# Kernel optimization log

Measured on AMD Instinct MI355X. Metric: run time of the kernel, lower is better.

## Reference

```python
import jax, jax.numpy as jnp
import numpy as np

L, B, D, V = 4096, 4, 512, 1000  # seq_len, batch, hidden_dim, index_dim


def setup_inputs() -> dict:
    key = jax.random.key(0)
    k0, k1, k2, k3, k4 = jax.random.split(key, 5)
    s_d = 1.0 / np.sqrt(D)
    return {
        "x": jax.random.normal(k0, (L, B, D), dtype=jnp.float32),
        # ctc_weight: nn.Linear(D, D)
        "Ww": jax.random.uniform(k1, (D, D), dtype=jnp.float32, minval=-s_d, maxval=s_d),
        "Wb": jax.random.uniform(k2, (D,), dtype=jnp.float32, minval=-s_d, maxval=s_d),
        # ctc_linear: nn.Linear(D, V)
        "Lw": jax.random.uniform(k3, (V, D), dtype=jnp.float32, minval=-s_d, maxval=s_d),
        "Lb": jax.random.uniform(k4, (V,), dtype=jnp.float32, minval=-s_d, maxval=s_d),
    }


def reference(x, Ww, Wb, Lw, Lb):
    # x: (L, B, D) -> (B, L, D)
    xb = jnp.transpose(x, (1, 0, 2))
    # ctc_weight(x): (B, L, D)
    wx = xb @ Ww.T + Wb
    # bmm(x, W(x)^T): (B, L, L) bilinear scores (no softmax)
    scores = jnp.einsum('bld,bmd->blm', xb, wx)
    # bmm(scores, x): (B, L, D)
    y = jnp.einsum('blm,bmd->bld', scores, xb)
    # ctc_linear + log_softmax over vocab
    logits = y @ Lw.T + Lb  # (B, L, V)
    out = jax.nn.log_softmax(logits, axis=2)
    # permute back to (L, B, V)
    return jnp.transpose(out, (1, 0, 2))
```

## Files before the change

### kernel.cpp

```cpp
#include <hip/hip_runtime.h>
#include <math.h>

#define L_ 4096
#define B_ 4
#define D_ 512
#define V_ 1000
#define VP 1024
#define BD 2048
#define OUT_BV 4000
#define NCH 8

typedef __attribute__((ext_vector_type(8))) short short8;
typedef __attribute__((ext_vector_type(4))) float f32x4;
typedef __attribute__((ext_vector_type(4))) short short4v;

__device__ __forceinline__ short f2bf(float f) {
  unsigned u = __float_as_uint(f);
  unsigned r = (u + 0x7FFFu + ((u >> 16) & 1u)) >> 16;
  return (short)r;
}
__device__ __forceinline__ float bf2f(short v) {
  return __uint_as_float(((unsigned)(unsigned short)v) << 16);
}

__global__ __launch_bounds__(256) void kPre(const float* __restrict__ x,
                                            const float* __restrict__ Wb,
                                            short* __restrict__ xbf,
                                            short* __restrict__ xT,
                                            float* __restrict__ s,
                                            float* __restrict__ c) {
  const int l0 = blockIdx.x * 64, d0 = blockIdx.y * 64, b = blockIdx.z;
  __shared__ short tile[64 * 72];
  const int tid = threadIdx.x;
  const int r = tid >> 2;
  const int q = tid & 3;
  const int c0 = q * 16;

  short sv[16];
  float cpart = 0.f;
  const float* src = x + (size_t)(l0 + r) * BD + b * D_ + d0 + c0;
#pragma unroll
  for (int qq = 0; qq < 4; ++qq) {
    float4 f = *(const float4*)(src + qq * 4);
    const float* wb = Wb + d0 + c0 + qq * 4;
    cpart += f.x * wb[0] + f.y * wb[1] + f.z * wb[2] + f.w * wb[3];
    sv[qq * 4 + 0] = f2bf(f.x); sv[qq * 4 + 1] = f2bf(f.y);
    sv[qq * 4 + 2] = f2bf(f.z); sv[qq * 4 + 3] = f2bf(f.w);
  }
  short* dst = xbf + ((size_t)b * L_ + l0 + r) * D_ + d0 + c0;
  *(short8*)(dst)     = *(short8*)(sv);
  *(short8*)(dst + 8) = *(short8*)(sv + 8);
#pragma unroll
  for (int i = 0; i < 16; ++i) tile[(c0 + i) * 72 + r] = sv[i];
  cpart += __shfl_xor(cpart, 1);
  cpart += __shfl_xor(cpart, 2);
  if (q == 0) atomicAdd(&c[b * L_ + l0 + r], cpart);
  __syncthreads();
  short8 t0 = *(const short8*)(tile + r * 72 + c0);
  short8 t1 = *(const short8*)(tile + r * 72 + c0 + 8);
  short* tdst = xT + ((size_t)b * D_ + d0 + r) * L_ + l0 + c0;
  *(short8*)(tdst)     = t0;
  *(short8*)(tdst + 8) = t1;
  float spart = 0.f;
#pragma unroll
  for (int i = 0; i < 8; ++i) spart += bf2f(t0[i]) + bf2f(t1[i]);
  spart += __shfl_xor(spart, 1);
  spart += __shfl_xor(spart, 2);
  if (q == 0) atomicAdd(&s[b * D_ + d0 + r], spart);
}

__global__ __launch_bounds__(256) void kT(const float* __restrict__ Lw,
                                          const float* __restrict__ s,
                                          float* __restrict__ t) {
  const int w = threadIdx.x >> 6, lane = threadIdx.x & 63;
  const int wid = blockIdx.x * 4 + w;
  const int b = wid >> 10, v = wid & 1023;
  float sum = 0.f;
  if (v < V_) {
    const float* lr = Lw + (size_t)v * D_;
    const float* sb = s + b * D_;
#pragma unroll
    for (int i = 0; i < 8; ++i) sum += lr[lane + i * 64] * sb[lane + i * 64];
  }
  for (int off = 32; off; off >>= 1) sum += __shfl_down(sum, off);
  if (lane == 0) t[b * VP + v] = (v < V_) ? sum : 0.f;
}

__global__ __launch_bounds__(256) void kGbf(const short* __restrict__ xT,
                                            short* __restrict__ Gpart) {
  const int z = blockIdx.z;
  const int b = z >> 3, ch = z & 7;
  const int i0 = blockIdx.x * 128, j0 = blockIdx.y * 128;
  const short* Ab = xT + (size_t)b * D_ * L_;
  __shared__ short As[128 * 64];
  __shared__ short Bs[128 * 64];
  f32x4 acc[4][4] = {};
  const int tid = threadIdx.x;
  const int w = tid >> 6, lane = tid & 63;
  const int quad = lane >> 4, mcol = lane & 15;
  const int wr0 = (w & 1) * 64, wc0 = (w >> 1) * 64;
  const int kbase = ch * 512;

  for (int k0 = kbase; k0 < kbase + 512; k0 += 64) {
#pragma unroll
    for (int q = 0; q < 4; ++q) {
      const int u = q * 256 + tid;
      const int row = u >> 3, blk = u & 7;
      const int phys = blk ^ (row & 7);
      *(short8*)(As + row * 64 + phys * 8) =
          *(const short8*)(Ab + (size_t)(i0 + row) * L_ + k0 + blk * 8);
      *(short8*)(Bs + row * 64 + phys * 8) =
          *(const short8*)(Ab + (size_t)(j0 + row) * L_ + k0 + blk * 8);
    }
    __syncthreads();
#pragma unroll
    for (int ss = 0; ss < 2; ++ss) {
      short8 af[4], bf[4];
#pragma unroll
      for (int i = 0; i < 4; ++i) {
        const int arow = wr0 + i * 16 + mcol;
        const int ablk = (ss * 4 + quad) ^ (arow & 7);
        af[i] = *(const short8*)(As + arow * 64 + ablk * 8);
        const int brow = wc0 + i * 16 + mcol;
        const int bblk = (ss * 4 + quad) ^ (brow & 7);
        bf[i] = *(const short8*)(Bs + brow * 64 + bblk * 8);
      }
#pragma unroll
      for (int i = 0; i < 4; ++i)
#pragma unroll
        for (int j = 0; j < 4; ++j)
          acc[i][j] = __builtin_amdgcn_mfma_f32_16x16x32_bf16(af[i], bf[j],
                                                              acc[i][j], 0, 0, 0);
    }
    __syncthreads();
  }
  short* Gp = Gpart + (size_t)z * (D_ * D_);
#pragma unroll
  for (int i = 0; i < 4; ++i)
#pragma unroll
    for (int j = 0; j < 4; ++j) {
      const int col = j0 + wc0 + j * 16 + mcol;
#pragma unroll
      for (int r = 0; r < 4; ++r) {
        const int rowi = i0 + wr0 + i * 16 + quad * 4 + r;
        Gp[(size_t)rowi * D_ + col] = f2bf(acc[i][j][r]);
      }
    }
}

__global__ __launch_bounds__(256) void kGredW(const short* __restrict__ Gpart,
                                              short* __restrict__ Gb,
                                              const float* __restrict__ Ww,
                                              const float* __restrict__ Lw,
                                              short* __restrict__ Wwb,
                                              short* __restrict__ Lwb) {
  if (blockIdx.x < 512) {
    const int idx = blockIdx.x * 256 + threadIdx.x;
    const int b = idx >> 15, e = (idx & 32767) * 8;
    float sum[8] = {};
#pragma unroll
    for (int ch = 0; ch < NCH; ++ch) {
      short8 v = *(const short8*)(Gpart + ((size_t)(b * NCH + ch)) * (D_ * D_) + e);
#pragma unroll
      for (int i = 0; i < 8; ++i) sum[i] += bf2f(v[i]);
    }
    short8 o;
#pragma unroll
    for (int i = 0; i < 8; ++i) o[i] = f2bf(sum[i]);
    *(short8*)(Gb + (size_t)b * (D_ * D_) + e) = o;
  } else {
    const int idx = (blockIdx.x - 512) * 256 + threadIdx.x;
    if (idx < 65536) {
      const int e = idx * 4;
      float4 f = *(const float4*)(Ww + e);
      short4v o; o[0] = f2bf(f.x); o[1] = f2bf(f.y); o[2] = f2bf(f.z); o[3] = f2bf(f.w);
      *(short4v*)(Wwb + e) = o;
    } else {
      const int e = (idx - 65536) * 4;
      const int v = e >> 9;
      short4v o = {};
      if (v < V_) {
        float4 f = *(const float4*)(Lw + e);
        o[0] = f2bf(f.x); o[1] = f2bf(f.y); o[2] = f2bf(f.z); o[3] = f2bf(f.w);
      }
      *(short4v*)(Lwb + e) = o;
    }
  }
}

__global__ __launch_bounds__(256) void kMbf64(const short* __restrict__ Wwb,
                                              const short* __restrict__ Gb,
                                              short* __restrict__ Mb) {
  const int b = blockIdx.z;
  const int i0 = blockIdx.x * 64, j0 = blockIdx.y * 64;
  const short* Bbase = Gb + (size_t)b * D_ * D_;
  __shared__ short As[64 * 64];
  __shared__ short Bs[64 * 64];
  f32x4 acc[2][2] = {};
  const int tid = threadIdx.x;
  const int w = tid >> 6, lane = tid & 63;
  const int quad = lane >> 4, mcol = lane & 15;
  const int wr0 = (w & 1) * 32, wc0 = (w >> 1) * 32;

  for (int k0 = 0; k0 < D_; k0 += 64) {
#pragma unroll
    for (int q = 0; q < 2; ++q) {
      const int u = q * 256 + tid;
      const int row = u >> 3, blk = u & 7;
      const int phys = blk ^ (row & 7);
      *(short8*)(As + row * 64 + phys * 8) =
          *(const short8*)(Wwb + (size_t)(i0 + row) * D_ + k0 + blk * 8);
      *(short8*)(Bs + row * 64 + phys * 8) =
          *(const short8*)(Bbase + (size_t)(j0 + row) * D_ + k0 + blk * 8);
    }
    __syncthreads();
#pragma unroll
    for (int ss = 0; ss < 2; ++ss) {
      short8 af[2], bf[2];
#pragma unroll
      for (int i = 0; i < 2; ++i) {
        const int arow = wr0 + i * 16 + mcol;
        const int ablk = (ss * 4 + quad) ^ (arow & 7);
        af[i] = *(const short8*)(As + arow * 64 + ablk * 8);
        const int brow = wc0 + i * 16 + mcol;
        const int bblk = (ss * 4 + quad) ^ (brow & 7);
        bf[i] = *(const short8*)(Bs + brow * 64 + bblk * 8);
      }
#pragma unroll
      for (int i = 0; i < 2; ++i)
#pragma unroll
        for (int j = 0; j < 2; ++j)
          acc[i][j] = __builtin_amdgcn_mfma_f32_16x16x32_bf16(af[i], bf[j],
                                                              acc[i][j], 0, 0, 0);
    }
    __syncthreads();
  }
  short* Mo = Mb + (size_t)b * D_ * D_;
#pragma unroll
  for (int i = 0; i < 2; ++i)
#pragma unroll
    for (int j = 0; j < 2; ++j) {
      const int col = j0 + wc0 + j * 16 + mcol;
#pragma unroll
      for (int r = 0; r < 4; ++r) {
        const int rowi = i0 + wr0 + i * 16 + quad * 4 + r;
        Mo[(size_t)rowi * D_ + col] = f2bf(acc[i][j][r]);
      }
    }
}

__global__ __launch_bounds__(256) void kPbf64(const short* __restrict__ Lwb,
                                              const short* __restrict__ Mb,
                                              short* __restrict__ Ptb) {
  const int b = blockIdx.z;
  const int i0 = blockIdx.x * 64;
  const int j0 = blockIdx.y * 64;
  const short* Bbase = Mb + (size_t)b * D_ * D_;
  __shared__ short As[64 * 64];
  __shared__ short Bs[64 * 64];
  f32x4 acc[2][2] = {};
  const int tid = threadIdx.x;
  const int w = tid >> 6, lane = tid & 63;
  const int quad = lane >> 4, mcol = lane & 15;
  const int wr0 = (w & 1) * 32, wc0 = (w >> 1) * 32;

  for (int k0 = 0; k0 < D_; k0 += 64) {
#pragma unroll
    for (int q = 0; q < 2; ++q) {
      const int u = q * 256 + tid;
      const int row = u >> 3, blk = u & 7;
      const int phys = blk ^ (row & 7);
      *(short8*)(As + row * 64 + phys * 8) =
          *(const short8*)(Lwb + (size_t)(i0 + row) * D_ + k0 + blk * 8);
      *(short8*)(Bs + row * 64 + phys * 8) =
          *(const short8*)(Bbase + (size_t)(j0 + row) * D_ + k0 + blk * 8);
    }
    __syncthreads();
#pragma unroll
    for (int ss = 0; ss < 2; ++ss) {
      short8 af[2], bf[2];
#pragma unroll
      for (int i = 0; i < 2; ++i) {
        const int arow = wr0 + i * 16 + mcol;
        const int ablk = (ss * 4 + quad) ^ (arow & 7);
        af[i] = *(const short8*)(As + arow * 64 + ablk * 8);
        const int brow = wc0 + i * 16 + mcol;
        const int bblk = (ss * 4 + quad) ^ (brow & 7);
        bf[i] = *(const short8*)(Bs + brow * 64 + bblk * 8);
      }
#pragma unroll
      for (int i = 0; i < 2; ++i)
#pragma unroll
        for (int j = 0; j < 2; ++j)
          acc[i][j] = __builtin_amdgcn_mfma_f32_16x16x32_bf16(af[i], bf[j],
                                                              acc[i][j], 0, 0, 0);
    }
    __syncthreads();
  }
  short* Po = Ptb + (size_t)b * VP * D_;
#pragma unroll
  for (int i = 0; i < 2; ++i)
#pragma unroll
    for (int j = 0; j < 2; ++j) {
      const int col = j0 + wc0 + j * 16 + mcol;
#pragma unroll
      for (int r = 0; r < 4; ++r) {
        const int rowi = i0 + wr0 + i * 16 + quad * 4 + r;
        Po[(size_t)rowi * D_ + col] = f2bf(acc[i][j][r]);
      }
    }
}

__global__ __launch_bounds__(256) void kLogits2(const short* __restrict__ xbf,
                                                const short* __restrict__ Ptb,
                                                const float* __restrict__ c,
                                                const float* __restrict__ t,
                                                const float* __restrict__ Lb,
                                                short* __restrict__ logitsBf) {
  const int b = blockIdx.z;
  const int l0t = blockIdx.x * 128;
  const int v0t = blockIdx.y * 128;
  const short* Abase = Ptb + (size_t)b * VP * D_;
  const short* Bbase = xbf + (size_t)b * L_ * D_;
  __shared__ short As[128 * 64];
  __shared__ short Bs[128 * 64];
  f32x4 acc[4][4] = {};
  const int tid = threadIdx.x;
  const int w = tid >> 6, lane = tid & 63;
  const int quad = lane >> 4, mcol = lane & 15;
  const int wr0 = (w & 1) * 64, wc0 = (w >> 1) * 64;

  for (int k0 = 0; k0 < D_; k0 += 64) {
#pragma unroll
    for (int q = 0; q < 4; ++q) {
      const int u = q * 256 + tid;
      const int row = u >> 3, blk = u & 7;
      const int phys = blk ^ (row & 7);
      *(short8*)(As + row * 64 + phys * 8) =
          *(const short8*)(Abase + (size_t)(v0t + row) * D_ + k0 + blk * 8);
      *(short8*)(Bs + row * 64 + phys * 8) =
          *(const short8*)(Bbase + (size_t)(l0t + row) * D_ + k0 + blk * 8);
    }
    __syncthreads();
#pragma unroll
    for (int ss = 0; ss < 2; ++ss) {
      short8 af[4], bf[4];
#pragma unroll
      for (int i = 0; i < 4; ++i) {
        const int arow = wr0 + i * 16 + mcol;
        const int ablk = (ss * 4 + quad) ^ (arow & 7);
        af[i] = *(const short8*)(As + arow * 64 + ablk * 8);
        const int brow = wc0 + i * 16 + mcol;
        const int bblk = (ss * 4 + quad) ^ (brow & 7);
        bf[i] = *(const short8*)(Bs + brow * 64 + bblk * 8);
      }
#pragma unroll
      for (int i = 0; i < 4; ++i)
#pragma unroll
        for (int j = 0; j < 4; ++j)
          acc[i][j] = __builtin_amdgcn_mfma_f32_16x16x32_bf16(af[i], bf[j],
                                                              acc[i][j], 0, 0, 0);
    }
    __syncthreads();
  }
#pragma unroll
  for (int j = 0; j < 4; ++j) {
    const int gl = l0t + wc0 + j * 16 + mcol;
    const float cl = c[b * L_ + gl];
#pragma unroll
    for (int i = 0; i < 4; ++i) {
      const int gv0 = v0t + wr0 + i * 16 + quad * 4;
      f32x4 tv = *(const f32x4*)(t + b * VP + gv0);
      f32x4 lb4 = {};
      if (gv0 < V_) lb4 = *(const f32x4*)(Lb + gv0);
      short4v o;
#pragma unroll
      for (int r = 0; r < 4; ++r)
        o[r] = f2bf(acc[i][j][r] + cl * tv[r] + lb4[r]);
      *(short4v*)(logitsBf + ((size_t)b * L_ + gl) * VP + gv0) = o;
    }
  }
}

__global__ __launch_bounds__(256) void kLsm(const short* __restrict__ logitsBf,
                                            float* __restrict__ out) {
  const int b = blockIdx.y;
  const int l = blockIdx.x * 4 + (threadIdx.x >> 6);
  const int lane = threadIdx.x & 63;
  const short* row = logitsBf + ((size_t)b * L_ + l) * VP;
  short8 v0 = *(const short8*)(row + lane * 16);
  short8 v1 = *(const short8*)(row + lane * 16 + 8);
  float vals[16];
#pragma unroll
  for (int i = 0; i < 8; ++i) { vals[i] = bf2f(v0[i]); vals[8 + i] = bf2f(v1[i]); }
  float m = -__builtin_inff();
#pragma unroll
  for (int i = 0; i < 16; ++i)
    if (lane * 16 + i < V_) m = fmaxf(m, vals[i]);
  for (int off = 32; off; off >>= 1) m = fmaxf(m, __shfl_xor(m, off));
  float se = 0.f;
#pragma unroll
  for (int i = 0; i < 16; ++i)
    if (lane * 16 + i < V_) se += expf(vals[i] - m);
  for (int off = 32; off; off >>= 1) se += __shfl_xor(se, off);
  const float lse = m + logf(se);
  float* orow = out + (size_t)l * OUT_BV + b * V_;
#pragma unroll
  for (int q = 0; q < 4; ++q) {
    const int base = lane * 16 + q * 4;
    if (base < V_) {
      float4 st = make_float4(vals[q * 4 + 0] - lse, vals[q * 4 + 1] - lse,
                              vals[q * 4 + 2] - lse, vals[q * 4 + 3] - lse);
      *(float4*)(orow + base) = st;
    }
  }
}

extern "C" void kernel_launch(void* const* d_in, const int* in_sizes, int n_in,
                              void* d_out, int out_size, void* d_ws,
                              size_t ws_size, hipStream_t stream) {
  const float* x  = (const float*)d_in[0];
  const float* Ww = (const float*)d_in[1];
  const float* Wb = (const float*)d_in[2];
  const float* Lw = (const float*)d_in[3];
  const float* Lb = (const float*)d_in[4];

  char* wp = (char*)d_ws;
  short* xbf = (short*)wp;   wp += (size_t)B_ * L_ * D_ * 2;
  short* xT  = (short*)wp;   wp += (size_t)B_ * L_ * D_ * 2;
  short* Ptb = (short*)wp;   wp += (size_t)B_ * VP * D_ * 2;
  short* Gpart = (short*)wp; wp += (size_t)B_ * NCH * D_ * D_ * 2;
  short* Gb  = (short*)wp;   wp += (size_t)B_ * D_ * D_ * 2;
  short* Mb  = (short*)wp;   wp += (size_t)B_ * D_ * D_ * 2;
  short* Wwb = (short*)wp;   wp += (size_t)D_ * D_ * 2;
  short* Lwb = (short*)wp;   wp += (size_t)VP * D_ * 2;
  float* s   = (float*)wp;   wp += (size_t)B_ * D_ * 4;
  float* c   = (float*)wp;   wp += (size_t)B_ * L_ * 4;
  float* t   = (float*)wp;   wp += (size_t)B_ * VP * 4;
  short* logitsBf = (short*)wp;

  hipMemsetAsync(s, 0, (size_t)(B_ * D_ + B_ * L_) * sizeof(float), stream);

  kPre<<<dim3(64, 8, B_), 256, 0, stream>>>(x, Wb, xbf, xT, s, c);
  kGbf<<<dim3(4, 4, B_ * NCH), 256, 0, stream>>>(xT, Gpart);
  kGredW<<<dim3(1280), 256, 0, stream>>>(Gpart, Gb, Ww, Lw, Wwb, Lwb);
  kMbf64<<<dim3(8, 8, B_), 256, 0, stream>>>(Wwb, Gb, Mb);
  kT<<<dim3(1024), 256, 0, stream>>>(Lw, s, t);
  kPbf64<<<dim3(16, 8, B_), 256, 0, stream>>>(Lwb, Mb, Ptb);
  kLogits2<<<dim3(32, 8, B_), 256, 0, stream>>>(xbf, Ptb, c, t, Lb, logitsBf);
  kLsm<<<dim3(L_ / 4, B_), 256, 0, stream>>>(logitsBf, (float*)d_out);
}
```

Before: 200.9 us.

## Use direct global-to-LDS loads, symmetric Gram tiles, and fuse kT into reduction

The Gram and logits GEMMs now load tiles with global_load_lds DMA instead of going through registers. To make that work, producers write xbf, xT and Ptb in a pre-swizzled XOR layout that matches the LDS bank-conflict pattern. The Gram kernel computes only the upper-triangle 128x128 tiles and mirrors them on store, and it doubles the K-split to 16 chunks to keep enough blocks in flight. The separate kT launch is folded into the reduction kernel. The trade-offs are twice as much partial-sum traffic in the reduction and scattered transposed stores for the mirrored tiles.

```diff
diff --git a/kernel.cpp b/kernel.cpp
--- a/kernel.cpp
+++ b/kernel.cpp
@@ -8,11 +8,18 @@
 #define VP 1024
 #define BD 2048
 #define OUT_BV 4000
-#define NCH 8
+#define NCH 16
 
 typedef __attribute__((ext_vector_type(8))) short short8;
 typedef __attribute__((ext_vector_type(4))) float f32x4;
 typedef __attribute__((ext_vector_type(4))) short short4v;
+
+typedef __attribute__((address_space(1))) const unsigned int gu32;
+typedef __attribute__((address_space(3))) unsigned int lu32;
+
+__device__ __forceinline__ void dma16(const void* g, void* l) {
+  __builtin_amdgcn_global_load_lds((gu32*)g, (lu32*)l, 16, 0, 0);
+}
 
 __device__ __forceinline__ short f2bf(float f) {
   unsigned u = __float_as_uint(f);
@@ -35,6 +42,8 @@
   const int r = tid >> 2;
   const int q = tid & 3;
   const int c0 = q * 16;
+  const int key = r & 7;
+  const int blk0 = c0 >> 3;
 
   short sv[16];
   float cpart = 0.f;
@@ -47,9 +56,9 @@
     sv[qq * 4 + 0] = f2bf(f.x); sv[qq * 4 + 1] = f2bf(f.y);
     sv[qq * 4 + 2] = f2bf(f.z); sv[qq * 4 + 3] = f2bf(f.w);
   }
-  short* dst = xbf + ((size_t)b * L_ + l0 + r) * D_ + d0 + c0;
-  *(short8*)(dst)     = *(short8*)(sv);
-  *(short8*)(dst + 8) = *(short8*)(sv + 8);
+  short* dst = xbf + ((size_t)b * L_ + l0 + r) * D_ + d0;
+  *(short8*)(dst + ((blk0 ^ key) * 8))       = *(short8*)(sv);
+  *(short8*)(dst + (((blk0 + 1) ^ key) * 8)) = *(short8*)(sv + 8);
 #pragma unroll
   for (int i = 0; i < 16; ++i) tile[(c0 + i) * 72 + r] = sv[i];
   cpart += __shfl_xor(cpart, 1);
@@ -58,9 +67,9 @@
   __syncthreads();
   short8 t0 = *(const short8*)(tile + r * 72 + c0);
   short8 t1 = *(const short8*)(tile + r * 72 + c0 + 8);
-  short* tdst = xT + ((size_t)b * D_ + d0 + r) * L_ + l0 + c0;
-  *(short8*)(tdst)     = t0;
-  *(short8*)(tdst + 8) = t1;
+  short* tdst = xT + ((size_t)b * D_ + d0 + r) * L_ + l0;
+  *(short8*)(tdst + ((blk0 ^ key) * 8))       = t0;
+  *(short8*)(tdst + (((blk0 + 1) ^ key) * 8)) = t1;
   float spart = 0.f;
 #pragma unroll
   for (int i = 0; i < 8; ++i) spart += bf2f(t0[i]) + bf2f(t1[i]);
@@ -69,28 +78,18 @@
   if (q == 0) atomicAdd(&s[b * D_ + d0 + r], spart);
 }
 
-__global__ __launch_bounds__(256) void kT(const float* __restrict__ Lw,
-                                          const float* __restrict__ s,
-                                          float* __restrict__ t) {
-  const int w = threadIdx.x >> 6, lane = threadIdx.x & 63;
-  const int wid = blockIdx.x * 4 + w;
-  const int b = wid >> 10, v = wid & 1023;
-  float sum = 0.f;
-  if (v < V_) {
-    const float* lr = Lw + (size_t)v * D_;
-    const float* sb = s + b * D_;
-#pragma unroll
-    for (int i = 0; i < 8; ++i) sum += lr[lane + i * 64] * sb[lane + i * 64];
-  }
-  for (int off = 32; off; off >>= 1) sum += __shfl_down(sum, off);
-  if (lane == 0) t[b * VP + v] = (v < V_) ? sum : 0.f;
-}
-
 __global__ __launch_bounds__(256) void kGbf(const short* __restrict__ xT,
                                             short* __restrict__ Gpart) {
   const int z = blockIdx.z;
-  const int b = z >> 3, ch = z & 7;
-  const int i0 = blockIdx.x * 128, j0 = blockIdx.y * 128;
+  const int b = z >> 4, ch = z & 15;
+  const int p = blockIdx.x;
+  int ti, tj;
+  if (p < 4)      { ti = 0; tj = p; }
+  else if (p < 7) { ti = 1; tj = p - 3; }
+  else if (p < 9) { ti = 2; tj = p - 5; }
+  else            { ti = 3; tj = 3; }
+  const int i0 = ti * 128, j0 = tj * 128;
+  const bool mirror = (ti != tj);
   const short* Ab = xT + (size_t)b * D_ * L_;
   __shared__ short As[128 * 64];
   __shared__ short Bs[128 * 64];
@@ -99,18 +98,16 @@
   const int w = tid >> 6, lane = tid & 63;
   const int quad = lane >> 4, mcol = lane & 15;
   const int wr0 = (w & 1) * 64, wc0 = (w >> 1) * 64;
-  const int kbase = ch * 512;
-
-  for (int k0 = kbase; k0 < kbase + 512; k0 += 64) {
-#pragma unroll
-    for (int q = 0; q < 4; ++q) {
-      const int u = q * 256 + tid;
-      const int row = u >> 3, blk = u & 7;
-      const int phys = blk ^ (row & 7);
-      *(short8*)(As + row * 64 + phys * 8) =
-          *(const short8*)(Ab + (size_t)(i0 + row) * L_ + k0 + blk * 8);
-      *(short8*)(Bs + row * 64 + phys * 8) =
-          *(const short8*)(Ab + (size_t)(j0 + row) * L_ + k0 + blk * 8);
+  const int kbase = ch * (L_ / NCH);
+
+  for (int k0 = kbase; k0 < kbase + (L_ / NCH); k0 += 64) {
+#pragma unroll
+    for (int t = 0; t < 4; ++t) {
+      const int cc = w * 4 + t;
+      const int gr = cc * 8 + (lane >> 3);
+      const int gc = k0 + (lane & 7) * 8;
+      dma16(Ab + (size_t)(i0 + gr) * L_ + gc, As + cc * 512);
+      dma16(Ab + (size_t)(j0 + gr) * L_ + gc, Bs + cc * 512);
     }
     __syncthreads();
 #pragma unroll
@@ -143,17 +140,21 @@
 #pragma unroll
       for (int r = 0; r < 4; ++r) {
         const int rowi = i0 + wr0 + i * 16 + quad * 4 + r;
-        Gp[(size_t)rowi * D_ + col] = f2bf(acc[i][j][r]);
-      }
-    }
-}
-
-__global__ __launch_bounds__(256) void kGredW(const short* __restrict__ Gpart,
-                                              short* __restrict__ Gb,
-                                              const float* __restrict__ Ww,
-                                              const float* __restrict__ Lw,
-                                              short* __restrict__ Wwb,
-                                              short* __restrict__ Lwb) {
+        const short v = f2bf(acc[i][j][r]);
+        Gp[(size_t)rowi * D_ + col] = v;
+        if (mirror) Gp[(size_t)col * D_ + rowi] = v;
+      }
+    }
+}
+
+__global__ __launch_bounds__(256) void kGredWT(const short* __restrict__ Gpart,
+                                               short* __restrict__ Gb,
+                                               const float* __restrict__ Ww,
+                                               const float* __restrict__ Lw,
+                                               short* __restrict__ Wwb,
+                                               short* __restrict__ Lwb,
+                                               const float* __restrict__ s,
+                                               float* __restrict__ t) {
   if (blockIdx.x < 512) {
     const int idx = blockIdx.x * 256 + threadIdx.x;
     const int b = idx >> 15, e = (idx & 32767) * 8;
@@ -168,7 +169,7 @@
 #pragma unroll
     for (int i = 0; i < 8; ++i) o[i] = f2bf(sum[i]);
     *(short8*)(Gb + (size_t)b * (D_ * D_) + e) = o;
-  } else {
+  } else if (blockIdx.x < 1280) {
     const int idx = (blockIdx.x - 512) * 256 + threadIdx.x;
     if (idx < 65536) {
       const int e = idx * 4;
@@ -185,6 +186,19 @@
       }
       *(short4v*)(Lwb + e) = o;
     }
+  } else {
+    const int w = threadIdx.x >> 6, lane = threadIdx.x & 63;
+    const int wid = (blockIdx.x - 1280) * 4 + w;
+    const int b = wid >> 10, v = wid & 1023;
+    float sum = 0.f;
+    if (v < V_) {
+      const float* lr = Lw + (size_t)v * D_;
+      const float* sb = s + b * D_;
+#pragma unroll
+      for (int i = 0; i < 8; ++i) sum += lr[lane + i * 64] * sb[lane + i * 64];
+    }
+    for (int off = 32; off; off >>= 1) sum += __shfl_down(sum, off);
+    if (lane == 0) t[b * VP + v] = (v < V_) ? sum : 0.f;
   }
 }
 
@@ -306,7 +320,9 @@
 #pragma unroll
       for (int r = 0; r < 4; ++r) {
         const int rowi = i0 + wr0 + i * 16 + quad * 4 + r;
-        Po[(size_t)rowi * D_ + col] = f2bf(acc[i][j][r]);
+        const int key = rowi & 7;
+        const int pcol = (col & ~63) | ((((col >> 3) & 7) ^ key) << 3) | (col & 7);
+        Po[(size_t)rowi * D_ + pcol] = f2bf(acc[i][j][r]);
       }
     }
 }
@@ -332,14 +348,12 @@
 
   for (int k0 = 0; k0 < D_; k0 += 64) {
 #pragma unroll
-    for (int q = 0; q < 4; ++q) {
-      const int u = q * 256 + tid;
-      const int row = u >> 3, blk = u & 7;
-      const int phys = blk ^ (row & 7);
-      *(short8*)(As + row * 64 + phys * 8) =
-          *(const short8*)(Abase + (size_t)(v0t + row) * D_ + k0 + blk * 8);
-      *(short8*)(Bs + row * 64 + phys * 8) =
-          *(const short8*)(Bbase + (size_t)(l0t + row) * D_ + k0 + blk * 8);
+    for (int t4 = 0; t4 < 4; ++t4) {
+      const int cc = w * 4 + t4;
+      const int gr = cc * 8 + (lane >> 3);
+      const int gc = k0 + (lane & 7) * 8;
+      dma16(Abase + (size_t)(v0t + gr) * D_ + gc, As + cc * 512);
+      dma16(Bbase + (size_t)(l0t + gr) * D_ + gc, Bs + cc * 512);
     }
     __syncthreads();
 #pragma unroll
@@ -442,10 +456,9 @@
   hipMemsetAsync(s, 0, (size_t)(B_ * D_ + B_ * L_) * sizeof(float), stream);
 
   kPre<<<dim3(64, 8, B_), 256, 0, stream>>>(x, Wb, xbf, xT, s, c);
-  kGbf<<<dim3(4, 4, B_ * NCH), 256, 0, stream>>>(xT, Gpart);
-  kGredW<<<dim3(1280), 256, 0, stream>>>(Gpart, Gb, Ww, Lw, Wwb, Lwb);
+  kGbf<<<dim3(10, 1, B_ * NCH), 256, 0, stream>>>(xT, Gpart);
+  kGredWT<<<dim3(2304), 256, 0, stream>>>(Gpart, Gb, Ww, Lw, Wwb, Lwb, s, t);
   kMbf64<<<dim3(8, 8, B_), 256, 0, stream>>>(Wwb, Gb, Mb);
-  kT<<<dim3(1024), 256, 0, stream>>>(Lw, s, t);
   kPbf64<<<dim3(16, 8, B_), 256, 0, stream>>>(Lwb, Mb, Ptb);
   kLogits2<<<dim3(32, 8, B_), 256, 0, stream>>>(xbf, Ptb, c, t, Lb, logitsBf);
   kLsm<<<dim3(L_ / 4, B_), 256, 0, stream>>>(logitsBf, (float*)d_out);
```

New measurement: 221.2 us. 10.1% more time.

## Pre-swizzle xbf and Ptb in global memory, DMA logits tiles directly to LDS

Applied to the files above, without the earlier changes.

The producers of xbf (kPre) and Ptb (kPbf64) now write each row in the XOR-swizzled 8-element block order that the logits kernel uses in LDS. The logits kernel can then use global_load_lds direct-to-LDS copies of 16 bytes per lane in place of loading into registers and storing to LDS. This is meant to cut VGPR traffic and instruction count in the main GEMM's staging. Separately, the small kT kernel is folded into the reduction/weight-conversion kernel as extra blocks, saving one launch. The risk is that the global swizzle layout must match exactly how the logits kernel reads the tiles.

```diff
diff --git a/kernel.cpp b/kernel.cpp
--- a/kernel.cpp
+++ b/kernel.cpp
@@ -13,6 +13,13 @@
 typedef __attribute__((ext_vector_type(8))) short short8;
 typedef __attribute__((ext_vector_type(4))) float f32x4;
 typedef __attribute__((ext_vector_type(4))) short short4v;
+
+typedef __attribute__((address_space(1))) const unsigned int gu32;
+typedef __attribute__((address_space(3))) unsigned int lu32;
+
+__device__ __forceinline__ void dma16(const void* g, void* l) {
+  __builtin_amdgcn_global_load_lds((gu32*)g, (lu32*)l, 16, 0, 0);
+}
 
 __device__ __forceinline__ short f2bf(float f) {
   unsigned u = __float_as_uint(f);
@@ -35,6 +42,8 @@
   const int r = tid >> 2;
   const int q = tid & 3;
   const int c0 = q * 16;
+  const int key = r & 7;
+  const int blk0 = c0 >> 3;
 
   short sv[16];
   float cpart = 0.f;
@@ -47,9 +56,9 @@
     sv[qq * 4 + 0] = f2bf(f.x); sv[qq * 4 + 1] = f2bf(f.y);
     sv[qq * 4 + 2] = f2bf(f.z); sv[qq * 4 + 3] = f2bf(f.w);
   }
-  short* dst = xbf + ((size_t)b * L_ + l0 + r) * D_ + d0 + c0;
-  *(short8*)(dst)     = *(short8*)(sv);
-  *(short8*)(dst + 8) = *(short8*)(sv + 8);
+  short* dst = xbf + ((size_t)b * L_ + l0 + r) * D_ + d0;
+  *(short8*)(dst + ((blk0 ^ key) * 8))       = *(short8*)(sv);
+  *(short8*)(dst + (((blk0 + 1) ^ key) * 8)) = *(short8*)(sv + 8);
 #pragma unroll
   for (int i = 0; i < 16; ++i) tile[(c0 + i) * 72 + r] = sv[i];
   cpart += __shfl_xor(cpart, 1);
@@ -67,23 +76,6 @@
   spart += __shfl_xor(spart, 1);
   spart += __shfl_xor(spart, 2);
   if (q == 0) atomicAdd(&s[b * D_ + d0 + r], spart);
-}
-
-__global__ __launch_bounds__(256) void kT(const float* __restrict__ Lw,
-                                          const float* __restrict__ s,
-                                          float* __restrict__ t) {
-  const int w = threadIdx.x >> 6, lane = threadIdx.x & 63;
-  const int wid = blockIdx.x * 4 + w;
-  const int b = wid >> 10, v = wid & 1023;
-  float sum = 0.f;
-  if (v < V_) {
-    const float* lr = Lw + (size_t)v * D_;
-    const float* sb = s + b * D_;
-#pragma unroll
-    for (int i = 0; i < 8; ++i) sum += lr[lane + i * 64] * sb[lane + i * 64];
-  }
-  for (int off = 32; off; off >>= 1) sum += __shfl_down(sum, off);
-  if (lane == 0) t[b * VP + v] = (v < V_) ? sum : 0.f;
 }
 
 __global__ __launch_bounds__(256) void kGbf(const short* __restrict__ xT,
@@ -148,12 +140,14 @@
     }
 }
 
-__global__ __launch_bounds__(256) void kGredW(const short* __restrict__ Gpart,
-                                              short* __restrict__ Gb,
-                                              const float* __restrict__ Ww,
-                                              const float* __restrict__ Lw,
-                                              short* __restrict__ Wwb,
-                                              short* __restrict__ Lwb) {
+__global__ __launch_bounds__(256) void kGredWT(const short* __restrict__ Gpart,
+                                               short* __restrict__ Gb,
+                                               const float* __restrict__ Ww,
+                                               const float* __restrict__ Lw,
+                                               short* __restrict__ Wwb,
+                                               short* __restrict__ Lwb,
+                                               const float* __restrict__ s,
+                                               float* __restrict__ t) {
   if (blockIdx.x < 512) {
     const int idx = blockIdx.x * 256 + threadIdx.x;
     const int b = idx >> 15, e = (idx & 32767) * 8;
@@ -168,7 +162,7 @@
 #pragma unroll
     for (int i = 0; i < 8; ++i) o[i] = f2bf(sum[i]);
     *(short8*)(Gb + (size_t)b * (D_ * D_) + e) = o;
-  } else {
+  } else if (blockIdx.x < 1280) {
     const int idx = (blockIdx.x - 512) * 256 + threadIdx.x;
     if (idx < 65536) {
       const int e = idx * 4;
@@ -185,6 +179,19 @@
       }
       *(short4v*)(Lwb + e) = o;
     }
+  } else {
+    const int w = threadIdx.x >> 6, lane = threadIdx.x & 63;
+    const int wid = (blockIdx.x - 1280) * 4 + w;
+    const int b = wid >> 10, v = wid & 1023;
+    float sum = 0.f;
+    if (v < V_) {
+      const float* lr = Lw + (size_t)v * D_;
+      const float* sb = s + b * D_;
+#pragma unroll
+      for (int i = 0; i < 8; ++i) sum += lr[lane + i * 64] * sb[lane + i * 64];
+    }
+    for (int off = 32; off; off >>= 1) sum += __shfl_down(sum, off);
+    if (lane == 0) t[b * VP + v] = (v < V_) ? sum : 0.f;
   }
 }
 
@@ -306,7 +313,9 @@
 #pragma unroll
       for (int r = 0; r < 4; ++r) {
         const int rowi = i0 + wr0 + i * 16 + quad * 4 + r;
-        Po[(size_t)rowi * D_ + col] = f2bf(acc[i][j][r]);
+        const int key = rowi & 7;
+        const int pcol = (col & ~63) | ((((col >> 3) & 7) ^ key) << 3) | (col & 7);
+        Po[(size_t)rowi * D_ + pcol] = f2bf(acc[i][j][r]);
       }
     }
 }
@@ -332,14 +341,12 @@
 
   for (int k0 = 0; k0 < D_; k0 += 64) {
 #pragma unroll
-    for (int q = 0; q < 4; ++q) {
-      const int u = q * 256 + tid;
-      const int row = u >> 3, blk = u & 7;
-      const int phys = blk ^ (row & 7);
-      *(short8*)(As + row * 64 + phys * 8) =
-          *(const short8*)(Abase + (size_t)(v0t + row) * D_ + k0 + blk * 8);
-      *(short8*)(Bs + row * 64 + phys * 8) =
-          *(const short8*)(Bbase + (size_t)(l0t + row) * D_ + k0 + blk * 8);
+    for (int t4 = 0; t4 < 4; ++t4) {
+      const int cc = w * 4 + t4;
+      const int gr = cc * 8 + (lane >> 3);
+      const int gc = k0 + (lane & 7) * 8;
+      dma16(Abase + (size_t)(v0t + gr) * D_ + gc, As + cc * 512);
+      dma16(Bbase + (size_t)(l0t + gr) * D_ + gc, Bs + cc * 512);
     }
     __syncthreads();
 #pragma unroll
@@ -443,9 +450,8 @@
 
   kPre<<<dim3(64, 8, B_), 256, 0, stream>>>(x, Wb, xbf, xT, s, c);
   kGbf<<<dim3(4, 4, B_ * NCH), 256, 0, stream>>>(xT, Gpart);
-  kGredW<<<dim3(1280), 256, 0, stream>>>(Gpart, Gb, Ww, Lw, Wwb, Lwb);
+  kGredWT<<<dim3(2304), 256, 0, stream>>>(Gpart, Gb, Ww, Lw, Wwb, Lwb, s, t);
   kMbf64<<<dim3(8, 8, B_), 256, 0, stream>>>(Wwb, Gb, Mb);
-  kT<<<dim3(1024), 256, 0, stream>>>(Lw, s, t);
   kPbf64<<<dim3(16, 8, B_), 256, 0, stream>>>(Lwb, Mb, Ptb);
   kLogits2<<<dim3(32, 8, B_), 256, 0, stream>>>(xbf, Ptb, c, t, Lb, logitsBf);
   kLsm<<<dim3(L_ / 4, B_), 256, 0, stream>>>(logitsBf, (float*)d_out);
```

Measured after the change: 199.3 us. No clear change (-0.8%).
